# Kernel tuning notes

Hardware: AMD Instinct MI355X
Metric: run time of the kernel (lower is better)

## Reference

```python
import jax, jax.numpy as jnp
import numpy as np

N_HASHES = 4
CHUNK = 144
REDUCTION = 4
RES_SCALE = 1.0
NORM_EPS = 5e-5


def conv2d(x, w, b, pad):
    y = jax.lax.conv_general_dilated(
        x, w, window_strides=(1, 1), padding=[(pad, pad), (pad, pad)],
        dimension_numbers=('NCHW', 'OIHW', 'NCHW'))
    return y + b[None, :, None, None]


def add_adjacent_buckets(x):
    # x: (N, h, n_chunks, chunk, e); concat each chunk with its circular neighbors
    back = jnp.roll(x, 1, axis=2)
    fwd = jnp.roll(x, -1, axis=2)
    return jnp.concatenate([x, back, fwd], axis=3)


def setup_inputs() -> dict:
    key = jax.random.key(0)
    ks = jax.random.split(key, 6)
    x = jax.random.normal(ks[0], (1, 32, 192, 192), jnp.float32)
    w_match = jax.random.normal(ks[1], (8, 32, 3, 3), jnp.float32) * 0.05
    b_match = jnp.zeros((8,), jnp.float32)
    w_asm = jax.random.normal(ks[2], (32, 32, 1, 1), jnp.float32) * 0.05
    b_asm = jnp.zeros((32,), jnp.float32)
    rotations = jax.random.normal(ks[3], (8, N_HASHES, 64), jnp.float32)
    return {'x': x, 'w_match': w_match, 'b_match': b_match,
            'w_asm': w_asm, 'b_asm': b_asm, 'rotations': rotations}


def reference(x, w_match, b_match, w_asm, b_asm, rotations):
    N, _, H, W = x.shape
    L = H * W
    # conv_match: 3x3 conv 32->8; conv_assembly: 1x1 conv 32->32
    x_embed = conv2d(x, w_match, b_match, 1).reshape(N, -1, L).transpose(0, 2, 1)  # (N, L, 8)
    y_embed = conv2d(x, w_asm, b_asm, 0).reshape(N, -1, L).transpose(0, 2, 1)      # (N, L, 32)
    C = x_embed.shape[-1]
    hash_buckets = min(L // CHUNK + (L // CHUNK) % 2, 128)  # = 128 here

    # --- LSH hashing (non-differentiable; rotations passed in for determinism) ---
    rotated = jnp.einsum('blf,fhi->bhli', x_embed, rotations)        # (N, h, L, hb/2)
    rotated = jnp.concatenate([rotated, -rotated], axis=-1)          # (N, h, L, hb)
    hash_codes = jnp.argmax(rotated, axis=-1)                        # (N, h, L)
    hash_codes = hash_codes + (jnp.arange(N_HASHES) * hash_buckets)[None, :, None]
    hash_codes = hash_codes.reshape(N, -1)                           # (N, h*L)

    # --- sort tokens by bucket id ---
    indices = jnp.argsort(hash_codes, axis=-1)
    undo_sort = jnp.argsort(indices, axis=-1)
    mod_indices = indices % L
    x_sorted = jnp.take_along_axis(x_embed, mod_indices[:, :, None], axis=1)  # (N, h*L, 8)
    y_sorted = jnp.take_along_axis(y_embed, mod_indices[:, :, None], axis=1)  # (N, h*L, 32)

    x_b = x_sorted.reshape(N, N_HASHES, -1, C)
    y_b = y_sorted.reshape(N, N_HASHES, -1, C * REDUCTION)
    padding = (-L) % CHUNK  # static; 0 for L=192*192
    if padding:
        x_b = jnp.concatenate([x_b, x_b[:, :, -padding:, :]], axis=2)
        y_b = jnp.concatenate([y_b, y_b[:, :, -padding:, :]], axis=2)
    x_b = x_b.reshape(N, N_HASHES, -1, CHUNK, C)
    y_b = y_b.reshape(N, N_HASHES, -1, CHUNK, C * REDUCTION)

    # --- bucketed attention with adjacent buckets ---
    nrm = jnp.linalg.norm(x_b, axis=-1, keepdims=True)
    x_match = x_b / jnp.maximum(nrm, NORM_EPS)   # F.normalize(eps=5e-5)
    x_match = add_adjacent_buckets(x_match)      # (N, h, k, 3*chunk, 8)
    y_adj = add_adjacent_buckets(y_b)            # (N, h, k, 3*chunk, 32)

    raw = jnp.einsum('bhkie,bhkje->bhkij', x_b, x_match)  # (N, h, k, 144, 432)
    bucket_score = jax.scipy.special.logsumexp(raw, axis=-1, keepdims=True)
    score = jnp.exp(raw - bucket_score)
    ret = jnp.einsum('bhkij,bhkje->bhkie', score, y_adj)  # (N, h, k, 144, 32)

    ret = ret.reshape(N, N_HASHES, -1, C * REDUCTION)
    bucket_score = bucket_score.reshape(N, N_HASHES, -1)
    if padding:
        ret = ret[:, :, :-padding, :]
        bucket_score = bucket_score[:, :, :-padding]
    ret = ret.reshape(N, -1, C * REDUCTION)
    bucket_score = bucket_score.reshape(N, -1)

    # --- unsort and combine hash rounds via softmax over logsumexp scores ---
    ret = jnp.take_along_axis(ret, undo_sort[:, :, None], axis=1)
    bucket_score = jnp.take_along_axis(bucket_score, undo_sort, axis=1)
    ret = ret.reshape(N, N_HASHES, L, C * REDUCTION)
    probs = jax.nn.softmax(bucket_score.reshape(N, N_HASHES, L, 1), axis=1)
    out = jnp.sum(ret * probs, axis=1)                     # (N, L, 32)
    out = out.transpose(0, 2, 1).reshape(N, -1, H, W) * RES_SCALE + x
    return out
```

## Files before the change

### kernel.cpp

```cpp
#include <hip/hip_runtime.h>
#include <hip/hip_bf16.h>
#include <math.h>

#define LTOT 36864
#define NH 4
#define NCHUNK 256
#define CHU 144
#define NBUCK 128
#define NSEG 144
#define HW_ 192
#define VTS 436

typedef unsigned int u32;
typedef unsigned short u16;
typedef unsigned long long u64;
typedef __attribute__((ext_vector_type(4))) short short4v;
typedef __attribute__((ext_vector_type(4))) float f32x4;

__device__ __forceinline__ u32 pkbf(float a, float b){
  union { __hip_bfloat162 h2; u32 u; } cv;
  cv.h2 = __float22bfloat162_rn(float2{a,b});
  return cv.u;
}
__device__ __forceinline__ float bflo(u32 w){ return __uint_as_float(w<<16); }
__device__ __forceinline__ float bfhi(u32 w){ return __uint_as_float(w & 0xffff0000u); }

__global__ __launch_bounds__(256) void k_conv(const float* __restrict__ x,
    const float* __restrict__ wm, const float* __restrict__ bm,
    const float* __restrict__ wa, const float* __restrict__ ba,
    float* __restrict__ xe, float* __restrict__ ye)
{
  __shared__ float xs[32*108];
  const int t = threadIdx.x;
  const int id = blockIdx.x;

  if (id < 576){
    const int bx = id % 12, by = id / 12;
    for (int idx=t; idx<3456; idx+=256){
      int ci = idx/108, rem = idx-ci*108;
      int iy = rem/18,  ix = rem-iy*18;
      int yy = by*4+iy-1, xx = bx*16+ix-1;
      float v = 0.f;
      if (yy>=0 && yy<HW_ && xx>=0 && xx<HW_) v = x[ci*LTOT + yy*HW_ + xx];
      xs[idx] = v;
    }
    __syncthreads();
    const int lane = t & 63;
    const int co0 = __builtin_amdgcn_readfirstlane((t>>6)<<1);
    const int ix = lane & 15, iy = lane >> 4;
    float a0 = bm[co0], a1 = bm[co0+1];
    const float* xb  = xs + iy*18 + ix;
    const float* w0p = wm + co0*288;
    const float* w1p = w0p + 288;
    for (int ci=0; ci<32; ci++){
      const float* xp = xb + ci*108;
      float x00=xp[0],  x01=xp[1],  x02=xp[2];
      float x10=xp[18], x11=xp[19], x12=xp[20];
      float x20=xp[36], x21=xp[37], x22=xp[38];
      const float* w0 = w0p + ci*9;
      const float* w1 = w1p + ci*9;
      a0 += x00*w0[0]+x01*w0[1]+x02*w0[2]
          + x10*w0[3]+x11*w0[4]+x12*w0[5]
          + x20*w0[6]+x21*w0[7]+x22*w0[8];
      a1 += x00*w1[0]+x01*w1[1]+x02*w1[2]
          + x10*w1[3]+x11*w1[4]+x12*w1[5]
          + x20*w1[6]+x21*w1[7]+x22*w1[8];
    }
    const int l = (by*4+iy)*HW_ + bx*16+ix;
    *(float2*)(xe + l*8 + co0) = float2{a0,a1};
  } else {
    const int zid = id - 576;
    const int cb = (zid/144)*8;
    const int l  = (zid%144)*256 + t;
    float acc[8];
    #pragma unroll
    for (int co=0;co<8;co++) acc[co] = ba[cb+co];
    #pragma unroll 4
    for (int ci=0; ci<32; ci++){
      float xv = x[ci*LTOT + l];
      #pragma unroll
      for (int co=0;co<8;co++) acc[co] += xv * wa[(cb+co)*32 + ci];
    }
    float4* yp = (float4*)(ye + l*32 + cb);
    yp[0] = make_float4(acc[0],acc[1],acc[2],acc[3]);
    yp[1] = make_float4(acc[4],acc[5],acc[6],acc[7]);
  }
}

__global__ __launch_bounds__(256) void k_hashrank(const float* __restrict__ xe,
    const float* __restrict__ rot, int* __restrict__ code,
    int* __restrict__ lrank, int* __restrict__ hist)
{
  const int h = blockIdx.y, seg = blockIdx.x, t = threadIdx.x;
  const int l = seg*256 + t;
  const float4* qp = (const float4*)(xe + l*8);
  float4 qa = qp[0], qb = qp[1];
  float best = -INFINITY; int bi = 0;
  float worst = INFINITY; int wi = 0;
  for (int i=0; i<64; i++){
    const float* rp = rot + h*64 + i;
    float v = qa.x*rp[0]    + qa.y*rp[256]  + qa.z*rp[512]  + qa.w*rp[768]
            + qb.x*rp[1024] + qb.y*rp[1280] + qb.z*rp[1536] + qb.w*rp[1792];
    if (v > best)  { best  = v; bi = i; }
    if (v < worst) { worst = v; wi = i; }
  }
  int c = (-worst > best) ? (64+wi) : bi;
  code[h*LTOT + l] = c;

  const int lane = t & 63, w = t >> 6;
  u64 mask = ~0ull;
  #pragma unroll
  for (int bit=0; bit<7; bit++){
    u64 bset = __ballot((c>>bit)&1);
    mask &= ((c>>bit)&1) ? bset : ~bset;
  }
  int rin = __popcll(mask & ((lane==0)?0ull:(~0ull >> (64-lane))));
  int cnt = __popcll(mask);

  __shared__ int wh[4][NBUCK];
  ((int*)wh)[t] = 0; ((int*)wh)[t+256] = 0;
  __syncthreads();
  if (rin == 0) wh[w][c] = cnt;
  __syncthreads();
  int r = rin;
  for (int ww=0; ww<w; ww++) r += wh[ww][c];
  lrank[h*LTOT + l] = r;
  if (t < NBUCK) hist[(h*NSEG+seg)*NBUCK + t] = wh[0][t]+wh[1][t]+wh[2][t]+wh[3][t];
}

__global__ __launch_bounds__(512) void k_scan(const int* __restrict__ hist,
    int* __restrict__ segoff)
{
  const int h = blockIdx.x;
  const int b = threadIdx.x & 127, g = threadIdx.x >> 7;
  int vals[36];
  int sum = 0;
  #pragma unroll
  for (int i=0;i<36;i++){
    vals[i] = hist[(h*NSEG + g*36 + i)*NBUCK + b];
    sum += vals[i];
  }
  __shared__ int ps[4][NBUCK];
  __shared__ int tot[NBUCK];
  __shared__ int scv[NBUCK];
  ps[g][b] = sum;
  __syncthreads();
  if (g == 0){
    int run = 0;
    #pragma unroll
    for (int gg=0; gg<4; gg++){ int tv = ps[gg][b]; ps[gg][b] = run; run += tv; }
    tot[b] = run;
    int v = run;
    #pragma unroll
    for (int off=1; off<64; off<<=1){
      int u = __shfl_up(v, off);
      if ((b & 63) >= off) v += u;
    }
    scv[b] = v;
  }
  __syncthreads();
  int base = scv[b] - tot[b] + ((b >= 64) ? scv[63] : 0);
  int run2 = base + ps[g][b];
  #pragma unroll
  for (int i=0;i<36;i++){
    segoff[(h*NSEG + g*36 + i)*NBUCK + b] = run2;
    run2 += vals[i];
  }
}

__global__ __launch_bounds__(256) void k_scatter(const int* __restrict__ code,
    const int* __restrict__ lrank, const int* __restrict__ segoff,
    const float* __restrict__ xe, const float* __restrict__ ye,
    int* __restrict__ rankof, u16* __restrict__ KQs, u16* __restrict__ Vs)
{
  const int h = blockIdx.y, seg = blockIdx.x, t = threadIdx.x;
  const int l = seg*256 + t;
  int c = code[h*LTOT + l];
  int r = segoff[(h*NSEG+seg)*NBUCK + c] + lrank[h*LTOT + l];
  rankof[h*LTOT + l] = r;

  const float4* xr = (const float4*)(xe + l*8);
  float4 a = xr[0], b = xr[1];
  float n2 = a.x*a.x+a.y*a.y+a.z*a.z+a.w*a.w
           + b.x*b.x+b.y*b.y+b.z*b.z+b.w*b.w;
  float sc = 1.0f / fmaxf(sqrtf(n2), 5e-5f);
  uint4 kq0, kq1;
  kq0.x = pkbf(a.x*sc,a.y*sc); kq0.y = pkbf(a.z*sc,a.w*sc);
  kq0.z = pkbf(b.x*sc,b.y*sc); kq0.w = pkbf(b.z*sc,b.w*sc);
  kq1.x = pkbf(a.x,a.y); kq1.y = pkbf(a.z,a.w);
  kq1.z = pkbf(b.x,b.y); kq1.w = pkbf(b.z,b.w);
  uint4* kqp = (uint4*)(KQs + (size_t)(h*LTOT + r)*16);
  kqp[0] = kq0; kqp[1] = kq1;

  const float4* yr = (const float4*)(ye + l*32);
  uint4* vp = (uint4*)(Vs + (size_t)(h*LTOT + r)*32);
  #pragma unroll
  for (int e4=0; e4<4; e4++){
    float4 v0 = yr[2*e4], v1 = yr[2*e4+1];
    uint4 w;
    w.x = pkbf(v0.x,v0.y); w.y = pkbf(v0.z,v0.w);
    w.z = pkbf(v1.x,v1.y); w.w = pkbf(v1.z,v1.w);
    vp[e4] = w;
  }
}

__global__ __launch_bounds__(576) void k_attn(const u16* __restrict__ KQs,
    const u16* __restrict__ Vs, u16* __restrict__ ret_s, float* __restrict__ bs_s)
{
  __shared__ __align__(16) u16 Klds[432*8];
  __shared__ __align__(16) u16 Qlds[144*8];
  __shared__ __align__(16) u16 VT[32*VTS];
  __shared__ float qn[CHU];

  const int t = threadIdx.x;
  const int k = blockIdx.x, h = blockIdx.y;
  const int base = ((k+NCHUNK-1)&(NCHUNK-1))*CHU;

  if (t < 432){
    int rr = base + t; if (rr >= LTOT) rr -= LTOT;
    *(uint4*)(Klds + t*8) = *(const uint4*)(KQs + (size_t)(h*LTOT+rr)*16);
  } else {
    int i = t - 432;
    uint4 qv = *(const uint4*)(KQs + (size_t)(h*LTOT + k*CHU + i)*16 + 8);
    *(uint4*)(Qlds + i*8) = qv;
    float f0=bflo(qv.x), f1=bfhi(qv.x), f2=bflo(qv.y), f3=bfhi(qv.y);
    float f4=bflo(qv.z), f5=bfhi(qv.z), f6=bflo(qv.w), f7=bfhi(qv.w);
    float n2 = f0*f0+f1*f1+f2*f2+f3*f3+f4*f4+f5*f5+f6*f6+f7*f7;
    qn[i] = sqrtf(n2)*1.01f + 1e-6f;
  }
  if (t < 432){
    int p = t >> 1, hf = t & 1;
    int rr = base + 2*p; if (rr >= LTOT) rr -= LTOT;
    const uint4* ra = (const uint4*)(Vs + (size_t)(h*LTOT+rr)*32);
    const uint4* rb = (const uint4*)(Vs + (size_t)(h*LTOT+rr+1)*32);
    uint4 A0 = ra[hf*2], A1 = ra[hf*2+1];
    uint4 B0 = rb[hf*2], B1 = rb[hf*2+1];
    u32 aw[8] = {A0.x,A0.y,A0.z,A0.w,A1.x,A1.y,A1.z,A1.w};
    u32 bw[8] = {B0.x,B0.y,B0.z,B0.w,B1.x,B1.y,B1.z,B1.w};
    int ebase = hf*16;
    #pragma unroll
    for (int m=0;m<8;m++){
      u32 al = aw[m]&0xffffu, ah = aw[m]>>16;
      u32 bl = bw[m]&0xffffu, bh = bw[m]>>16;
      *(u32*)&VT[(ebase+2*m  )*VTS + 2*p] = al | (bl<<16);
      *(u32*)&VT[(ebase+2*m+1)*VTS + 2*p] = ah | (bh<<16);
    }
  }
  __syncthreads();

  const int lane = t & 63;
  const int wv = t >> 6;
  const int q = lane & 15;
  const int quad = lane >> 4;

  const short4v zs = {0,0,0,0};
  short4v bq = zs;
  if (quad < 2) bq = *(const short4v*)(Qlds + (wv*16+q)*8 + quad*4);
  const float m = qn[wv*16+q];

  f32x4 o0 = {0.f,0.f,0.f,0.f}, o1 = {0.f,0.f,0.f,0.f};
  float s = 0.f;

  for (int kt=0; kt<27; kt++){
    short4v av = zs;
    if (quad < 2) av = *(const short4v*)(Klds + (kt*16+q)*8 + quad*4);
    f32x4 zc = {0.f,0.f,0.f,0.f};
    f32x4 st = __builtin_amdgcn_mfma_f32_16x16x16bf16_1k(av, bq, zc, 0,0,0);

    float p0 = __expf(st[0]-m), p1 = __expf(st[1]-m);
    float p2 = __expf(st[2]-m), p3 = __expf(st[3]-m);
    s += (p0+p1)+(p2+p3);

    union { u32 u[2]; short4v s4; } pk;
    pk.u[0] = pkbf(p0,p1);
    pk.u[1] = pkbf(p2,p3);

    short4v va0 = *(const short4v*)(&VT[ q    *VTS + kt*16 + quad*4]);
    short4v va1 = *(const short4v*)(&VT[(q+16)*VTS + kt*16 + quad*4]);
    o0 = __builtin_amdgcn_mfma_f32_16x16x16bf16_1k(va0, pk.s4, o0, 0,0,0);
    o1 = __builtin_amdgcn_mfma_f32_16x16x16bf16_1k(va1, pk.s4, o1, 0,0,0);
  }

  float stot = s;
  stot += __shfl_xor(stot, 16);
  stot += __shfl_xor(stot, 32);
  float inv = 1.0f / stot;

  const int row = h*LTOT + k*CHU + wv*16 + q;
  u16* rp = ret_s + (size_t)row*32;
  uint2 wA, wB;
  wA.x = pkbf(o0[0]*inv, o0[1]*inv); wA.y = pkbf(o0[2]*inv, o0[3]*inv);
  wB.x = pkbf(o1[0]*inv, o1[1]*inv); wB.y = pkbf(o1[2]*inv, o1[3]*inv);
  *(uint2*)&rp[quad*4]    = wA;
  *(uint2*)&rp[16+quad*4] = wB;
  if (lane < 16)
    bs_s[h*LTOT + k*CHU + wv*16 + lane] = m + __logf(stot);
}

__global__ __launch_bounds__(256) void k_final(const float* __restrict__ x,
    const int* __restrict__ rankof, const u16* __restrict__ ret_s,
    const float* __restrict__ bs_s, float* __restrict__ out)
{
  const int l  = blockIdx.x*64 + (threadIdx.x & 63);
  const int eg = threadIdx.x >> 6;
  int r[NH]; float bs[NH];
  #pragma unroll
  for (int h=0;h<NH;h++) r[h] = rankof[h*LTOT + l];
  #pragma unroll
  for (int h=0;h<NH;h++) bs[h] = bs_s[h*LTOT + r[h]];
  float m = fmaxf(fmaxf(bs[0],bs[1]), fmaxf(bs[2],bs[3]));
  float p[NH]; float s = 0.f;
  #pragma unroll
  for (int h=0;h<NH;h++){ p[h] = __expf(bs[h]-m); s += p[h]; }
  float inv = 1.0f/s;
  float o[8];
  #pragma unroll
  for (int e=0;e<8;e++) o[e]=0.f;
  #pragma unroll
  for (int h=0;h<NH;h++){
    float w = p[h]*inv;
    uint4 v = *(const uint4*)(ret_s + (size_t)(h*LTOT + r[h])*32 + eg*8);
    o[0] += w*bflo(v.x); o[1] += w*bfhi(v.x);
    o[2] += w*bflo(v.y); o[3] += w*bfhi(v.y);
    o[4] += w*bflo(v.z); o[5] += w*bfhi(v.z);
    o[6] += w*bflo(v.w); o[7] += w*bfhi(v.w);
  }
  #pragma unroll
  for (int e=0;e<8;e++){
    int ge = eg*8 + e;
    out[ge*LTOT + l] = o[e] + x[ge*LTOT + l];
  }
}

extern "C" void kernel_launch(void* const* d_in, const int* in_sizes, int n_in,
                              void* d_out, int out_size, void* d_ws, size_t ws_size,
                              hipStream_t stream)
{
  const float* x   = (const float*)d_in[0];
  const float* wm  = (const float*)d_in[1];
  const float* bm  = (const float*)d_in[2];
  const float* wa  = (const float*)d_in[3];
  const float* ba  = (const float*)d_in[4];
  const float* rot = (const float*)d_in[5];
  float* out = (float*)d_out;

  char* ws = (char*)d_ws;
  size_t off = 0;
  auto alloc = [&](size_t bytes)->void*{
    void* p = ws + off;
    off = (off + bytes + 255) & ~(size_t)255;
    return p;
  };
  float* xe     = (float*)alloc((size_t)LTOT*8*4);
  float* ye     = (float*)alloc((size_t)LTOT*32*4);
  int*   code   = (int*)  alloc((size_t)NH*LTOT*4);
  int*   lrank  = (int*)  alloc((size_t)NH*LTOT*4);
  int*   hist   = (int*)  alloc((size_t)NH*NSEG*NBUCK*4);
  int*   segoff = (int*)  alloc((size_t)NH*NSEG*NBUCK*4);
  int*   rankof = (int*)  alloc((size_t)NH*LTOT*4);
  u16*   KQs    = (u16*)  alloc((size_t)NH*LTOT*16*2);
  u16*   Vs     = (u16*)  alloc((size_t)NH*LTOT*32*2);
  u16*   ret_s  = (u16*)  alloc((size_t)NH*LTOT*32*2);
  float* bs_s   = (float*)alloc((size_t)NH*LTOT*4);

  hipLaunchKernelGGL(k_conv,     dim3(1152),       dim3(256), 0, stream, x, wm, bm, wa, ba, xe, ye);
  hipLaunchKernelGGL(k_hashrank, dim3(NSEG,NH),    dim3(256), 0, stream, xe, rot, code, lrank, hist);
  hipLaunchKernelGGL(k_scan,     dim3(NH),         dim3(512), 0, stream, hist, segoff);
  hipLaunchKernelGGL(k_scatter,  dim3(NSEG,NH),    dim3(256), 0, stream, code, lrank, segoff, xe, ye, rankof, KQs, Vs);
  hipLaunchKernelGGL(k_attn,     dim3(NCHUNK,NH),  dim3(576), 0, stream, KQs, Vs, ret_s, bs_s);
  hipLaunchKernelGGL(k_final,    dim3(576),        dim3(256), 0, stream, x, rankof, ret_s, bs_s, out);
}
```

Before: 145.1 us.

## Restructure LSH attention to stream neighbor chunks and give each wave two query tiles

The attention kernel drops from 9 waves with one query tile each to 5 waves, each handling two query tiles. The last wave duplicates tile 8. K/V for the three adjacent chunks are now loaded one chunk at a time into smaller LDS buffers, which cuts shared memory per block and should allow more resident blocks. Each loaded K and V fragment is reused across two query tiles. K and Q are stored in separate arrays so each kernel reads only what it needs. The trade-off is extra syncs per chunk, the redundant duplicate tile in the last wave, and fewer threads available to hide load latency.

```diff
diff --git a/kernel.cpp b/kernel.cpp
--- a/kernel.cpp
+++ b/kernel.cpp
@@ -9,7 +9,7 @@
 #define NBUCK 128
 #define NSEG 144
 #define HW_ 192
-#define VTS 436
+#define VTS 148
 
 typedef unsigned int u32;
 typedef unsigned short u16;
@@ -171,7 +171,8 @@
 __global__ __launch_bounds__(256) void k_scatter(const int* __restrict__ code,
     const int* __restrict__ lrank, const int* __restrict__ segoff,
     const float* __restrict__ xe, const float* __restrict__ ye,
-    int* __restrict__ rankof, u16* __restrict__ KQs, u16* __restrict__ Vs)
+    int* __restrict__ rankof, u16* __restrict__ Ks, u16* __restrict__ Qs,
+    u16* __restrict__ Vs)
 {
   const int h = blockIdx.y, seg = blockIdx.x, t = threadIdx.x;
   const int l = seg*256 + t;
@@ -184,13 +185,13 @@
   float n2 = a.x*a.x+a.y*a.y+a.z*a.z+a.w*a.w
            + b.x*b.x+b.y*b.y+b.z*b.z+b.w*b.w;
   float sc = 1.0f / fmaxf(sqrtf(n2), 5e-5f);
-  uint4 kq0, kq1;
-  kq0.x = pkbf(a.x*sc,a.y*sc); kq0.y = pkbf(a.z*sc,a.w*sc);
-  kq0.z = pkbf(b.x*sc,b.y*sc); kq0.w = pkbf(b.z*sc,b.w*sc);
-  kq1.x = pkbf(a.x,a.y); kq1.y = pkbf(a.z,a.w);
-  kq1.z = pkbf(b.x,b.y); kq1.w = pkbf(b.z,b.w);
-  uint4* kqp = (uint4*)(KQs + (size_t)(h*LTOT + r)*16);
-  kqp[0] = kq0; kqp[1] = kq1;
+  uint4 kk, qq;
+  kk.x = pkbf(a.x*sc,a.y*sc); kk.y = pkbf(a.z*sc,a.w*sc);
+  kk.z = pkbf(b.x*sc,b.y*sc); kk.w = pkbf(b.z*sc,b.w*sc);
+  qq.x = pkbf(a.x,a.y); qq.y = pkbf(a.z,a.w);
+  qq.z = pkbf(b.x,b.y); qq.w = pkbf(b.z,b.w);
+  *(uint4*)(Ks + (size_t)(h*LTOT + r)*8) = kk;
+  *(uint4*)(Qs + (size_t)(h*LTOT + r)*8) = qq;
 
   const float4* yr = (const float4*)(ye + l*32);
   uint4* vp = (uint4*)(Vs + (size_t)(h*LTOT + r)*32);
@@ -204,47 +205,25 @@
   }
 }
 
-__global__ __launch_bounds__(576) void k_attn(const u16* __restrict__ KQs,
-    const u16* __restrict__ Vs, u16* __restrict__ ret_s, float* __restrict__ bs_s)
-{
-  __shared__ __align__(16) u16 Klds[432*8];
-  __shared__ __align__(16) u16 Qlds[144*8];
+__global__ __launch_bounds__(320) void k_attn(const u16* __restrict__ Ks,
+    const u16* __restrict__ Qs, const u16* __restrict__ Vs,
+    u16* __restrict__ ret_s, float* __restrict__ bs_s)
+{
+  __shared__ __align__(16) u16 Klds[CHU*8];
+  __shared__ __align__(16) u16 Qlds[CHU*8];
   __shared__ __align__(16) u16 VT[32*VTS];
   __shared__ float qn[CHU];
 
   const int t = threadIdx.x;
   const int k = blockIdx.x, h = blockIdx.y;
-  const int base = ((k+NCHUNK-1)&(NCHUNK-1))*CHU;
-
-  if (t < 432){
-    int rr = base + t; if (rr >= LTOT) rr -= LTOT;
-    *(uint4*)(Klds + t*8) = *(const uint4*)(KQs + (size_t)(h*LTOT+rr)*16);
-  } else {
-    int i = t - 432;
-    uint4 qv = *(const uint4*)(KQs + (size_t)(h*LTOT + k*CHU + i)*16 + 8);
-    *(uint4*)(Qlds + i*8) = qv;
+
+  if (t < CHU){
+    uint4 qv = *(const uint4*)(Qs + (size_t)(h*LTOT + k*CHU + t)*8);
+    *(uint4*)(Qlds + t*8) = qv;
     float f0=bflo(qv.x), f1=bfhi(qv.x), f2=bflo(qv.y), f3=bfhi(qv.y);
     float f4=bflo(qv.z), f5=bfhi(qv.z), f6=bflo(qv.w), f7=bfhi(qv.w);
     float n2 = f0*f0+f1*f1+f2*f2+f3*f3+f4*f4+f5*f5+f6*f6+f7*f7;
-    qn[i] = sqrtf(n2)*1.01f + 1e-6f;
-  }
-  if (t < 432){
-    int p = t >> 1, hf = t & 1;
-    int rr = base + 2*p; if (rr >= LTOT) rr -= LTOT;
-    const uint4* ra = (const uint4*)(Vs + (size_t)(h*LTOT+rr)*32);
-    const uint4* rb = (const uint4*)(Vs + (size_t)(h*LTOT+rr+1)*32);
-    uint4 A0 = ra[hf*2], A1 = ra[hf*2+1];
-    uint4 B0 = rb[hf*2], B1 = rb[hf*2+1];
-    u32 aw[8] = {A0.x,A0.y,A0.z,A0.w,A1.x,A1.y,A1.z,A1.w};
-    u32 bw[8] = {B0.x,B0.y,B0.z,B0.w,B1.x,B1.y,B1.z,B1.w};
-    int ebase = hf*16;
-    #pragma unroll
-    for (int m=0;m<8;m++){
-      u32 al = aw[m]&0xffffu, ah = aw[m]>>16;
-      u32 bl = bw[m]&0xffffu, bh = bw[m]>>16;
-      *(u32*)&VT[(ebase+2*m  )*VTS + 2*p] = al | (bl<<16);
-      *(u32*)&VT[(ebase+2*m+1)*VTS + 2*p] = ah | (bh<<16);
-    }
+    qn[t] = sqrtf(n2)*1.01f + 1e-6f;
   }
   __syncthreads();
 
@@ -252,49 +231,94 @@
   const int wv = t >> 6;
   const int q = lane & 15;
   const int quad = lane >> 4;
+  const int tl0 = 2*wv, tl1 = (2*wv+1 < 9) ? 2*wv+1 : 8;
 
   const short4v zs = {0,0,0,0};
-  short4v bq = zs;
-  if (quad < 2) bq = *(const short4v*)(Qlds + (wv*16+q)*8 + quad*4);
-  const float m = qn[wv*16+q];
-
-  f32x4 o0 = {0.f,0.f,0.f,0.f}, o1 = {0.f,0.f,0.f,0.f};
-  float s = 0.f;
-
-  for (int kt=0; kt<27; kt++){
-    short4v av = zs;
-    if (quad < 2) av = *(const short4v*)(Klds + (kt*16+q)*8 + quad*4);
-    f32x4 zc = {0.f,0.f,0.f,0.f};
-    f32x4 st = __builtin_amdgcn_mfma_f32_16x16x16bf16_1k(av, bq, zc, 0,0,0);
-
-    float p0 = __expf(st[0]-m), p1 = __expf(st[1]-m);
-    float p2 = __expf(st[2]-m), p3 = __expf(st[3]-m);
-    s += (p0+p1)+(p2+p3);
-
-    union { u32 u[2]; short4v s4; } pk;
-    pk.u[0] = pkbf(p0,p1);
-    pk.u[1] = pkbf(p2,p3);
-
-    short4v va0 = *(const short4v*)(&VT[ q    *VTS + kt*16 + quad*4]);
-    short4v va1 = *(const short4v*)(&VT[(q+16)*VTS + kt*16 + quad*4]);
-    o0 = __builtin_amdgcn_mfma_f32_16x16x16bf16_1k(va0, pk.s4, o0, 0,0,0);
-    o1 = __builtin_amdgcn_mfma_f32_16x16x16bf16_1k(va1, pk.s4, o1, 0,0,0);
-  }
-
-  float stot = s;
-  stot += __shfl_xor(stot, 16);
-  stot += __shfl_xor(stot, 32);
-  float inv = 1.0f / stot;
-
-  const int row = h*LTOT + k*CHU + wv*16 + q;
-  u16* rp = ret_s + (size_t)row*32;
+  short4v bq0 = zs, bq1 = zs;
+  if (quad < 2){
+    bq0 = *(const short4v*)(Qlds + (tl0*16+q)*8 + quad*4);
+    bq1 = *(const short4v*)(Qlds + (tl1*16+q)*8 + quad*4);
+  }
+  const float m0 = qn[tl0*16+q], m1 = qn[tl1*16+q];
+
+  f32x4 o00={0,0,0,0}, o01={0,0,0,0}, o10={0,0,0,0}, o11={0,0,0,0};
+  float s0 = 0.f, s1 = 0.f;
+
+  for (int r=0; r<3; r++){
+    __syncthreads();
+    const int gkb = ((k + NCHUNK-1 + r) & (NCHUNK-1)) * CHU;
+    if (t < CHU){
+      *(uint4*)(Klds + t*8) = *(const uint4*)(Ks + (size_t)(h*LTOT + gkb + t)*8);
+    } else if (t >= 176){
+      int i = t - 176;
+      int p = i >> 1, hf = i & 1;
+      const uint4* ra = (const uint4*)(Vs + (size_t)(h*LTOT + gkb + 2*p)*32);
+      const uint4* rb = (const uint4*)(Vs + (size_t)(h*LTOT + gkb + 2*p+1)*32);
+      uint4 A0 = ra[hf*2], A1 = ra[hf*2+1];
+      uint4 B0 = rb[hf*2], B1 = rb[hf*2+1];
+      u32 aw[8] = {A0.x,A0.y,A0.z,A0.w,A1.x,A1.y,A1.z,A1.w};
+      u32 bw[8] = {B0.x,B0.y,B0.z,B0.w,B1.x,B1.y,B1.z,B1.w};
+      int ebase = hf*16;
+      #pragma unroll
+      for (int m=0;m<8;m++){
+        u32 al = aw[m]&0xffffu, ah = aw[m]>>16;
+        u32 bl = bw[m]&0xffffu, bh = bw[m]>>16;
+        *(u32*)&VT[(ebase+2*m  )*VTS + 2*p] = al | (bl<<16);
+        *(u32*)&VT[(ebase+2*m+1)*VTS + 2*p] = ah | (bh<<16);
+      }
+    }
+    __syncthreads();
+
+    #pragma unroll 3
+    for (int kt=0; kt<9; kt++){
+      short4v av = zs;
+      if (quad < 2) av = *(const short4v*)(Klds + (kt*16+q)*8 + quad*4);
+      f32x4 zc = {0.f,0.f,0.f,0.f};
+      f32x4 stA = __builtin_amdgcn_mfma_f32_16x16x16bf16_1k(av, bq0, zc, 0,0,0);
+      f32x4 stB = __builtin_amdgcn_mfma_f32_16x16x16bf16_1k(av, bq1, zc, 0,0,0);
+
+      float pA0 = __expf(stA[0]-m0), pA1 = __expf(stA[1]-m0);
+      float pA2 = __expf(stA[2]-m0), pA3 = __expf(stA[3]-m0);
+      float pB0 = __expf(stB[0]-m1), pB1 = __expf(stB[1]-m1);
+      float pB2 = __expf(stB[2]-m1), pB3 = __expf(stB[3]-m1);
+      s0 += (pA0+pA1)+(pA2+pA3);
+      s1 += (pB0+pB1)+(pB2+pB3);
+
+      union { u32 u[2]; short4v s4; } pkA, pkB;
+      pkA.u[0] = pkbf(pA0,pA1); pkA.u[1] = pkbf(pA2,pA3);
+      pkB.u[0] = pkbf(pB0,pB1); pkB.u[1] = pkbf(pB2,pB3);
+
+      short4v va0 = *(const short4v*)(&VT[ q    *VTS + kt*16 + quad*4]);
+      short4v va1 = *(const short4v*)(&VT[(q+16)*VTS + kt*16 + quad*4]);
+      o00 = __builtin_amdgcn_mfma_f32_16x16x16bf16_1k(va0, pkA.s4, o00, 0,0,0);
+      o01 = __builtin_amdgcn_mfma_f32_16x16x16bf16_1k(va1, pkA.s4, o01, 0,0,0);
+      o10 = __builtin_amdgcn_mfma_f32_16x16x16bf16_1k(va0, pkB.s4, o10, 0,0,0);
+      o11 = __builtin_amdgcn_mfma_f32_16x16x16bf16_1k(va1, pkB.s4, o11, 0,0,0);
+    }
+  }
+
+  float st0 = s0, st1 = s1;
+  st0 += __shfl_xor(st0, 16); st0 += __shfl_xor(st0, 32);
+  st1 += __shfl_xor(st1, 16); st1 += __shfl_xor(st1, 32);
+  float inv0 = 1.0f/st0, inv1 = 1.0f/st1;
+
+  const int row0 = h*LTOT + k*CHU + tl0*16 + q;
+  const int row1 = h*LTOT + k*CHU + tl1*16 + q;
+  u16* rp0 = ret_s + (size_t)row0*32;
+  u16* rp1 = ret_s + (size_t)row1*32;
   uint2 wA, wB;
-  wA.x = pkbf(o0[0]*inv, o0[1]*inv); wA.y = pkbf(o0[2]*inv, o0[3]*inv);
-  wB.x = pkbf(o1[0]*inv, o1[1]*inv); wB.y = pkbf(o1[2]*inv, o1[3]*inv);
-  *(uint2*)&rp[quad*4]    = wA;
-  *(uint2*)&rp[16+quad*4] = wB;
-  if (lane < 16)
-    bs_s[h*LTOT + k*CHU + wv*16 + lane] = m + __logf(stot);
+  wA.x = pkbf(o00[0]*inv0, o00[1]*inv0); wA.y = pkbf(o00[2]*inv0, o00[3]*inv0);
+  wB.x = pkbf(o01[0]*inv0, o01[1]*inv0); wB.y = pkbf(o01[2]*inv0, o01[3]*inv0);
+  *(uint2*)&rp0[quad*4]    = wA;
+  *(uint2*)&rp0[16+quad*4] = wB;
+  wA.x = pkbf(o10[0]*inv1, o10[1]*inv1); wA.y = pkbf(o10[2]*inv1, o10[3]*inv1);
+  wB.x = pkbf(o11[0]*inv1, o11[1]*inv1); wB.y = pkbf(o11[2]*inv1, o11[3]*inv1);
+  *(uint2*)&rp1[quad*4]    = wA;
+  *(uint2*)&rp1[16+quad*4] = wB;
+  if (quad == 0){
+    bs_s[row0] = m0 + __logf(st0);
+    bs_s[row1] = m1 + __logf(st1);
+  }
 }
 
 __global__ __launch_bounds__(256) void k_final(const float* __restrict__ x,
@@ -358,7 +382,8 @@
   int*   hist   = (int*)  alloc((size_t)NH*NSEG*NBUCK*4);
   int*   segoff = (int*)  alloc((size_t)NH*NSEG*NBUCK*4);
   int*   rankof = (int*)  alloc((size_t)NH*LTOT*4);
-  u16*   KQs    = (u16*)  alloc((size_t)NH*LTOT*16*2);
+  u16*   Ks     = (u16*)  alloc((size_t)NH*LTOT*8*2);
+  u16*   Qs     = (u16*)  alloc((size_t)NH*LTOT*8*2);
   u16*   Vs     = (u16*)  alloc((size_t)NH*LTOT*32*2);
   u16*   ret_s  = (u16*)  alloc((size_t)NH*LTOT*32*2);
   float* bs_s   = (float*)alloc((size_t)NH*LTOT*4);
@@ -366,7 +391,7 @@
   hipLaunchKernelGGL(k_conv,     dim3(1152),       dim3(256), 0, stream, x, wm, bm, wa, ba, xe, ye);
   hipLaunchKernelGGL(k_hashrank, dim3(NSEG,NH),    dim3(256), 0, stream, xe, rot, code, lrank, hist);
   hipLaunchKernelGGL(k_scan,     dim3(NH),         dim3(512), 0, stream, hist, segoff);
-  hipLaunchKernelGGL(k_scatter,  dim3(NSEG,NH),    dim3(256), 0, stream, code, lrank, segoff, xe, ye, rankof, KQs, Vs);
-  hipLaunchKernelGGL(k_attn,     dim3(NCHUNK,NH),  dim3(576), 0, stream, KQs, Vs, ret_s, bs_s);
+  hipLaunchKernelGGL(k_scatter,  dim3(NSEG,NH),    dim3(256), 0, stream, code, lrank, segoff, xe, ye, rankof, Ks, Qs, Vs);
+  hipLaunchKernelGGL(k_attn,     dim3(NCHUNK,NH),  dim3(320), 0, stream, Ks, Qs, Vs, ret_s, bs_s);
   hipLaunchKernelGGL(k_final,    dim3(576),        dim3(256), 0, stream, x, rankof, ret_s, bs_s, out);
 }
```

Measured after the change: 137.5 us. 5.2% less time.
